# Optimization experiments

Measured on AMD Instinct MI355X. Metric: run time of the kernel, lower is better.

Reference implementation:

```python
import jax, jax.numpy as jnp
import numpy as np

N_NODES = 100_000
N_EDGES = 1_600_000
N_GRAPHS = 64
EPS = 1e-7  # GENConv message epsilon
D_IN, D_H, D_OUT, OUT_DIM = 128, 192, 128, 10


def _w(k, fan_in, fan_out):
    return jax.random.normal(k, (fan_in, fan_out), jnp.float32) * (1.0 / np.sqrt(fan_in))


def setup_inputs() -> dict:
    key = jax.random.key(0)
    ks = jax.random.split(key, 8)
    return {
        "x": jax.random.normal(ks[0], (N_NODES, D_IN), jnp.float32),
        "W0": _w(ks[1], D_IN, D_H), "b0": jnp.zeros((D_H,), jnp.float32),
        "W1": _w(ks[2], D_H, D_H), "b1": jnp.zeros((D_H,), jnp.float32),
        "W2": _w(ks[3], D_H, D_H), "b2": jnp.zeros((D_H,), jnp.float32),
        "W3": _w(ks[4], D_H, D_OUT), "b3": jnp.zeros((D_OUT,), jnp.float32),
        "Wfc": _w(ks[5], D_OUT, OUT_DIM), "bfc": jnp.zeros((OUT_DIM,), jnp.float32),
        "edge_index": jax.random.randint(ks[6], (2, N_EDGES), 0, N_NODES, jnp.int32),
        "batch": jnp.sort(jax.random.randint(ks[7], (N_NODES,), 0, N_GRAPHS, jnp.int32)),
    }


def _genconv(x, W, b, src, dst):
    # GENConv (num_layers=1, aggr='add'): message = relu(x_j) + eps,
    # scatter-add to dst, residual add, single Linear MLP.
    msg = jax.nn.relu(x[src]) + EPS          # [E, d]
    agg = jax.ops.segment_sum(msg, dst, num_segments=N_NODES)  # [N, d]
    return (x + agg) @ W + b


def reference(x, W0, b0, W1, b1, W2, b2, W3, b3, Wfc, bfc, edge_index, batch):
    src, dst = edge_index[0], edge_index[1]  # source_to_target flow
    for W, b in ((W0, b0), (W1, b1), (W2, b2), (W3, b3)):
        x = _genconv(x, W, b, src, dst)
    # global mean pool over graphs
    sums = jax.ops.segment_sum(x, batch, num_segments=N_GRAPHS)
    counts = jax.ops.segment_sum(jnp.ones((x.shape[0],), x.dtype), batch,
                                 num_segments=N_GRAPHS)
    pooled = sums / jnp.maximum(counts, 1.0)[:, None]  # [G, D_OUT]
    logits = pooled @ Wfc + bfc                        # [G, OUT_DIM]
    return jax.nn.log_softmax(logits, axis=1)
```

## Files before the change

### kernel.cpp

```cpp
#include <hip/hip_runtime.h>
#include <hip/hip_bf16.h>
#include <stdint.h>

constexpr int NN = 100000;
constexpr int NE = 1600000;
constexpr int NG = 64;
constexpr int S  = 192;
constexpr int NB_SCAN = 98;
constexpr unsigned int ZOFF = (unsigned int)NN * 384u;

constexpr int PREP_CONVX_BLK = 12500;
constexpr int PREP_INDEG_BLK = 1563;
constexpr int PREP_CONVW_BLK = 384;
constexpr int PREP_GB_BLK    = 391;
constexpr int PREP_GRID = PREP_CONVX_BLK + PREP_INDEG_BLK + PREP_CONVW_BLK + PREP_GB_BLK;

constexpr int EG_BLOCKS = 391;
constexpr int HROW = 50048;

typedef __bf16 bf16x8 __attribute__((ext_vector_type(8)));
typedef float  f32x16 __attribute__((ext_vector_type(16)));
typedef float  f32x2  __attribute__((ext_vector_type(2)));

union U16x4 { uint4 u; bf16x8 b; };

__device__ __forceinline__ float bl(unsigned int u) { return __uint_as_float(u << 16); }
__device__ __forceinline__ float bh(unsigned int u) { return __uint_as_float(u & 0xffff0000u); }
__device__ __forceinline__ float b16f(unsigned short u) { return __uint_as_float(((unsigned int)u) << 16); }
__device__ __forceinline__ unsigned int fb(float f) {
    unsigned int u = __float_as_uint(f);
    return (u + 0x7fffu + ((u >> 16) & 1u)) >> 16;
}
__device__ __forceinline__ unsigned int prelu(unsigned int u) {
    unsigned int r;
    asm("v_pk_max_f16 %0, %1, %2" : "=v"(r) : "v"(u), "v"(0u));
    return r;
}
__device__ __forceinline__ unsigned int cnt2bf(unsigned int h) {
    float f0 = (float)(h & 0xffffu);
    float f1 = (float)(h >> 16);
    return (__float_as_uint(f0) >> 16) | (__float_as_uint(f1) & 0xffff0000u);
}

__global__ __launch_bounds__(256) void k_prep(const float* __restrict__ x,
                                              const int* __restrict__ ei,
                                              const int* __restrict__ bat,
                                              const float* __restrict__ W0, const float* __restrict__ W1,
                                              const float* __restrict__ W2,
                                              unsigned short* __restrict__ A_,
                                              int* __restrict__ indeg, int* __restrict__ slot,
                                              unsigned short* __restrict__ T0, unsigned short* __restrict__ T1,
                                              unsigned short* __restrict__ T2,
                                              int* __restrict__ nstart) {
    const int b = blockIdx.x;
    if (b < PREP_CONVX_BLK) {
        int id = b * 256 + threadIdx.x;
        if (id < 96) ((unsigned int*)(A_ + (size_t)NN * S))[id] = 0u;
        int row = id >> 5, c4 = id & 31;
        float4 v = ((const float4*)x)[id];
        uint2 a;
        a.x = fb(v.x) | (fb(v.y) << 16);
        a.y = fb(v.z) | (fb(v.w) << 16);
        *(uint2*)(A_ + row * S + c4 * 4) = a;
    } else if (b < PREP_CONVX_BLK + PREP_INDEG_BLK) {
        int e4 = ((b - PREP_CONVX_BLK) * 256 + threadIdx.x) * 4;
        if (e4 < NE) {
            int4 d = *(const int4*)(ei + NE + e4);
            int4 sl;
            sl.x = atomicAdd(&indeg[d.x], 1);
            sl.y = atomicAdd(&indeg[d.y], 1);
            sl.z = atomicAdd(&indeg[d.z], 1);
            sl.w = atomicAdd(&indeg[d.w], 1);
            *(int4*)(slot + e4) = sl;
        }
    } else if (b < PREP_CONVX_BLK + PREP_INDEG_BLK + PREP_CONVW_BLK) {
        int id = (b - PREP_CONVX_BLK - PREP_INDEG_BLK) * 256 + threadIdx.x;
        const float* W; unsigned short* T; int N, base;
        if      (id < 24576) { W = W0; T = T0; N = 192; base = 0;     }
        else if (id < 61440) { W = W1; T = T1; N = 192; base = 24576; }
        else                 { W = W2; T = T2; N = 192; base = 61440; }
        int lid = id - base;
        int ci = lid >> 3, j = lid & 7;
        int kc = ci / N, n = ci % N;
        T[lid] = (unsigned short)fb(W[(kc * 8 + j) * N + n]);
    } else {
        int n = (b - PREP_CONVX_BLK - PREP_INDEG_BLK - PREP_CONVW_BLK) * 256 + threadIdx.x;
        if (n < NN) {
            int b0 = bat[n];
            int bprev = (n == 0) ? -1 : bat[n - 1];
            for (int g = bprev + 1; g <= b0; g++) nstart[g] = n;
            if (n == NN - 1)
                for (int g = b0 + 1; g < NG; g++) nstart[g] = NN;
        }
    }
}

__global__ __launch_bounds__(1024) void k_scan1(const int* __restrict__ indeg, int* __restrict__ offs,
                                                int* __restrict__ partials) {
    __shared__ int s[1024];
    int t = threadIdx.x;
    int gid = blockIdx.x * 1024 + t;
    int v = (gid < NN) ? indeg[gid] : 0;
    s[t] = v;
    __syncthreads();
    for (int d = 1; d < 1024; d <<= 1) {
        int tv = (t >= d) ? s[t - d] : 0;
        __syncthreads();
        s[t] += tv;
        __syncthreads();
    }
    if (gid < NN) offs[gid + 1] = s[t];
    if (t == 1023) partials[blockIdx.x] = s[1023];
}

__global__ __launch_bounds__(128) void k_scan2(int* __restrict__ offs, int* __restrict__ partials) {
    __shared__ int s[128];
    int t = threadIdx.x;
    int v = (t < NB_SCAN) ? partials[t] : 0;
    s[t] = v;
    __syncthreads();
    for (int d = 1; d < 128; d <<= 1) {
        int tv = (t >= d) ? s[t - d] : 0;
        __syncthreads();
        s[t] += tv;
        __syncthreads();
    }
    if (t < NB_SCAN) partials[t] = s[t] - v;
    if (t == 0) offs[0] = 0;
}

__global__ __launch_bounds__(1024) void k_scan3(int* __restrict__ offs, const int* __restrict__ partials) {
    int gid = blockIdx.x * 1024 + threadIdx.x;
    if (gid < NN) offs[gid + 1] += partials[blockIdx.x];
}

__global__ __launch_bounds__(256) void k_fill(const int* __restrict__ ei, const int* __restrict__ offs,
                                              const int* __restrict__ slot, int* __restrict__ csr) {
    int e4 = (blockIdx.x * 256 + threadIdx.x) * 4;
    if (e4 >= NE) return;
    int4 sv = *(const int4*)(ei + e4);
    int4 dv = *(const int4*)(ei + NE + e4);
    int4 sl = *(const int4*)(slot + e4);
    csr[offs[dv.x] + sl.x] = sv.x;
    csr[offs[dv.y] + sl.y] = sv.y;
    csr[offs[dv.z] + sl.z] = sv.z;
    csr[offs[dv.w] + sl.w] = sv.w;
}

__global__ __launch_bounds__(256, 8) void k_agg192(const unsigned short* __restrict__ Ain,
                                                   unsigned short* __restrict__ Yout,
                                                   const int* __restrict__ offs,
                                                   const int* __restrict__ indeg,
                                                   const int* __restrict__ csr) {
    const int w = threadIdx.x >> 6, lane = threadIdx.x & 63;
    const int i = __builtin_amdgcn_readfirstlane(blockIdx.x * 4 + w);
    const bool act = lane < 48;
    const int deg   = __builtin_amdgcn_readfirstlane(indeg[i]);
    const int start = __builtin_amdgcn_readfirstlane(offs[i]);
    const int fo = (act ? lane : 47) * 8;
    const char* Ab = (const char*)Ain;

    f32x2 A01, A23;
    {
        uint2 p = *(const uint2*)(Ab + (size_t)i * 384 + fo);
        const float ed = 1e-7f * (float)deg;
        A01 = (f32x2){bl(p.x) + ed, bh(p.x) + ed};
        A23 = (f32x2){bl(p.y) + ed, bh(p.y) + ed};
    }

    const int* ecsr = csr + start;
    for (int e = 0; e < deg; e += 16) {
        unsigned int off[16];
#pragma unroll
        for (int k = 0; k < 16; k++) {
            int v = ecsr[e + k];
            off[k] = (e + k < deg) ? (unsigned int)v * 384u : ZOFF;
        }
        uint2 p[16];
#pragma unroll
        for (int k = 0; k < 16; k++)
            p[k] = *(const uint2*)(Ab + (size_t)off[k] + fo);
#pragma unroll
        for (int k = 0; k < 16; k++) {
            unsigned int rx = prelu(p[k].x), ry = prelu(p[k].y);
            A01 += (f32x2){bl(rx), bh(rx)};
            A23 += (f32x2){bl(ry), bh(ry)};
        }
    }
    if (act) {
        uint2 o;
        o.x = fb(A01.x) | (fb(A01.y) << 16);
        o.y = fb(A23.x) | (fb(A23.y) << 16);
        *(uint2*)(Yout + (size_t)i * S + lane * 4) = o;
    }
}

__global__ __launch_bounds__(256, 8) void k_agg128(const unsigned short* __restrict__ Ain,
                                                   unsigned short* __restrict__ Yout,
                                                   const int* __restrict__ offs,
                                                   const int* __restrict__ indeg,
                                                   const int* __restrict__ csr) {
    const int w = threadIdx.x >> 6, lane = threadIdx.x & 63;
    const int i = __builtin_amdgcn_readfirstlane(blockIdx.x * 4 + w);
    const int deg   = __builtin_amdgcn_readfirstlane(indeg[i]);
    const int start = __builtin_amdgcn_readfirstlane(offs[i]);
    const int fo = lane * 4;
    const char* Ab = (const char*)Ain;

    f32x2 A01;
    {
        unsigned int p = *(const unsigned int*)(Ab + (size_t)i * 384 + fo);
        const float ed = 1e-7f * (float)deg;
        A01 = (f32x2){bl(p) + ed, bh(p) + ed};
    }

    const int* ecsr = csr + start;
    for (int e = 0; e < deg; e += 16) {
        unsigned int off[16];
#pragma unroll
        for (int k = 0; k < 16; k++) {
            int v = ecsr[e + k];
            off[k] = (e + k < deg) ? (unsigned int)v * 384u : ZOFF;
        }
        unsigned int q[16];
#pragma unroll
        for (int k = 0; k < 16; k++)
            q[k] = *(const unsigned int*)(Ab + (size_t)off[k] + fo);
#pragma unroll
        for (int k = 0; k < 16; k++) {
            unsigned int r = prelu(q[k]);
            A01 += (f32x2){bl(r), bh(r)};
        }
    }
    *(unsigned int*)(Yout + (size_t)i * S + lane * 2) =
        fb(A01.x) | (fb(A01.y) << 16);
}

template <int K, int N>
__global__ __launch_bounds__(256) void k_gemm(const unsigned short* __restrict__ Yin,
                                              const unsigned short* __restrict__ WtC,
                                              const float* __restrict__ bias,
                                              unsigned short* __restrict__ Aout) {
    static_assert(K % 16 == 0 && N % 32 == 0, "");
    const int w = threadIdx.x >> 6, lane = threadIdx.x & 63;
    const int rt = blockIdx.x * 4 + w;
    if (rt >= (NN / 32)) return;
    const int hl = lane >> 5, lr = lane & 31;
    const int row0 = rt * 32;
    f32x16 acc[N / 32];
#pragma unroll
    for (int c = 0; c < N / 32; c++)
#pragma unroll
        for (int r = 0; r < 16; r++) acc[c][r] = 0.f;

    const unsigned short* ap = Yin + (row0 + lr) * S + hl * 8;
    const uint4* b4 = (const uint4*)WtC;
#pragma unroll
    for (int ks = 0; ks < K / 16; ks++) {
        U16x4 a;
        a.u = *(const uint4*)(ap + ks * 16);
#pragma unroll
        for (int c = 0; c < N / 32; c++) {
            U16x4 b;
            b.u = b4[(ks * 2 + hl) * N + c * 32 + lr];
            acc[c] = __builtin_amdgcn_mfma_f32_32x32x16_bf16(a.b, b.b, acc[c], 0, 0, 0);
        }
    }
#pragma unroll
    for (int c = 0; c < N / 32; c++) {
        const int col = c * 32 + lr;
        const float bc = bias[col];
#pragma unroll
        for (int r = 0; r < 16; r++) {
            const int row = row0 + (r & 3) + 8 * (r >> 2) + 4 * hl;
            Aout[row * S + col] = (unsigned short)fb(acc[c][r] + bc);
        }
    }
}

__global__ __launch_bounds__(1024) void k_hist(const int* __restrict__ csr, const int* __restrict__ offs,
                                               const int* __restrict__ nstart,
                                               unsigned int* __restrict__ hist) {
    const int g = blockIdx.x;
    unsigned int* hrow = hist + (size_t)g * HROW;
    for (int i = threadIdx.x; i < HROW; i += 1024) hrow[i] = 0u;
    __syncthreads();
    const int s0 = offs[nstart[g]];
    const int s1 = (g == NG - 1) ? NE : offs[nstart[g + 1]];
    for (int p = s0 + threadIdx.x; p < s1; p += 1024) {
        int src = csr[p];
        atomicAdd(&hrow[src >> 1], 1u << (16 * (src & 1)));
    }
}

__global__ __launch_bounds__(384) void k_egemm(const unsigned short* __restrict__ A0,
                                               const unsigned int* __restrict__ hist,
                                               float* __restrict__ partials) {
    const int wv = threadIdx.x >> 6, lane = threadIdx.x & 63;
    const int b = blockIdx.x;
    const int j0 = b * 256;
    const int hl = lane >> 5, lr = lane & 31;
    const int feat = wv * 32 + lr;
    f32x16 acc[2];
#pragma unroll
    for (int m = 0; m < 2; m++)
#pragma unroll
        for (int r = 0; r < 16; r++) acc[m][r] = 0.f;

    for (int kk = 0; kk < 16; kk++) {
        const int jh = (j0 >> 1) + kk * 8 + hl * 4;
        U16x4 af[2];
#pragma unroll
        for (int m = 0; m < 2; m++) {
            uint4 h = *(const uint4*)(hist + (size_t)(m * 32 + lr) * HROW + jh);
            af[m].u = (uint4){cnt2bf(h.x), cnt2bf(h.y), cnt2bf(h.z), cnt2bf(h.w)};
        }
        U16x4 bf;
#pragma unroll
        for (int tp = 0; tp < 4; tp++) {
            int je = j0 + kk * 16 + hl * 8 + tp * 2;
            int ja = min(je, NN), jb = min(je + 1, NN);
            unsigned int u0 = A0[(size_t)ja * S + feat];
            unsigned int u1 = A0[(size_t)jb * S + feat];
            ((unsigned int*)&bf.u)[tp] = prelu(u0 | (u1 << 16));
        }
#pragma unroll
        for (int m = 0; m < 2; m++)
            acc[m] = __builtin_amdgcn_mfma_f32_32x32x16_bf16(af[m].b, bf.b, acc[m], 0, 0, 0);
    }
    float* pb = partials + (size_t)b * 12288;
#pragma unroll
    for (int m = 0; m < 2; m++)
#pragma unroll
        for (int r = 0; r < 16; r++) {
            const int g = m * 32 + (r & 3) + 8 * (r >> 2) + 4 * hl;
            pb[g * 192 + feat] = acc[m][r];
        }
}

__global__ __launch_bounds__(256) void k_reduce(const float* __restrict__ partials,
                                                float* __restrict__ msg) {
    int gf = blockIdx.x * 256 + threadIdx.x;
    if (gf >= 12288) return;
    float s = 0.f;
    for (int p = 0; p < EG_BLOCKS; p++)
        s += partials[(size_t)p * 12288 + gf];
    msg[gf] = s;
}

__global__ __launch_bounds__(192) void k_pool(const unsigned short* __restrict__ A_,
                                              const int* __restrict__ batch,
                                              const int* __restrict__ indeg,
                                              float* __restrict__ sums, float* __restrict__ cnt,
                                              float* __restrict__ degsum) {
    const int b = blockIdx.x;
    const int f = threadIdx.x;
    int n0 = b * 200;
    int n1 = min(n0 + 200, NN);
    int cur = batch[n0];
    float acc = 0.f;
    int run = 0, dacc = 0;
    for (int n = n0; n < n1; n++) {
        int g = batch[n];
        if (g != cur) {
            atomicAdd(&sums[cur * 192 + f], acc);
            if (f == 0) { atomicAdd(&cnt[cur], (float)run); atomicAdd(&degsum[cur], (float)dacc); }
            acc = 0.f; run = 0; dacc = 0; cur = g;
        }
        acc += b16f(A_[(size_t)n * S + f]);
        run++;
        if (f == 0) dacc += indeg[n];
    }
    atomicAdd(&sums[cur * 192 + f], acc);
    if (f == 0) { atomicAdd(&cnt[cur], (float)run); atomicAdd(&degsum[cur], (float)dacc); }
}

__global__ __launch_bounds__(128) void k_head(const float* __restrict__ sums, const float* __restrict__ msg,
                                              const float* __restrict__ cnt, const float* __restrict__ degsum,
                                              const float* __restrict__ W3, const float* __restrict__ b3,
                                              const float* __restrict__ Wfc, const float* __restrict__ bfc,
                                              float* __restrict__ out) {
    __shared__ float py[192];
    __shared__ float tl[128];
    __shared__ float lg[10];
    const int g = blockIdx.x, t = threadIdx.x;
    const float inv = 1.f / fmaxf(cnt[g], 1.f);
    const float ed = 1e-7f * degsum[g];
    for (int k = t; k < 192; k += 128)
        py[k] = (sums[g * 192 + k] + msg[g * 192 + k] + ed) * inv;
    __syncthreads();
    float tf = b3[t];
    for (int k = 0; k < 192; k++) tf += py[k] * W3[k * 128 + t];
    tl[t] = tf;
    __syncthreads();
    if (t < 10) {
        float s = bfc[t];
        for (int f = 0; f < 128; f++) s += tl[f] * Wfc[f * 10 + t];
        lg[t] = s;
    }
    __syncthreads();
    if (t < 10) {
        float m = lg[0];
        for (int k = 1; k < 10; k++) m = fmaxf(m, lg[k]);
        float se = 0.f;
        for (int k = 0; k < 10; k++) se += expf(lg[k] - m);
        out[g * 10 + t] = lg[t] - m - logf(se);
    }
}

constexpr size_t A0_OFF     = 0;
constexpr size_t A1_OFF     = 38400384;
constexpr size_t HIST_REL   = 0;
constexpr size_t PARTS_REL  = 12812288;
constexpr size_t CSR_OFF    = 76800384;
constexpr size_t OFFS_OFF   = 83200384;
constexpr size_t INDEG_OFF  = 83600512;
constexpr size_t SUMS_OFF   = 84000512;
constexpr size_t CNT_OFF    = 84049664;
constexpr size_t DEGS_OFF   = 84049920;
constexpr size_t PART_OFF   = 84050176;
constexpr size_t NSTART_OFF = 84050688;
constexpr size_t WT0_OFF    = 84050944;
constexpr size_t WT1_OFF    = 84100096;
constexpr size_t WT2_OFF    = 84173824;
constexpr size_t MSG_OFF    = 84247552;

extern "C" void kernel_launch(void* const* d_in, const int* in_sizes, int n_in,
                              void* d_out, int out_size, void* d_ws, size_t ws_size,
                              hipStream_t stream) {
    const float* x   = (const float*)d_in[0];
    const float* W0  = (const float*)d_in[1];
    const float* b0  = (const float*)d_in[2];
    const float* W1  = (const float*)d_in[3];
    const float* b1  = (const float*)d_in[4];
    const float* W2  = (const float*)d_in[5];
    const float* b2  = (const float*)d_in[6];
    const float* W3  = (const float*)d_in[7];
    const float* b3  = (const float*)d_in[8];
    const float* Wfc = (const float*)d_in[9];
    const float* bfc = (const float*)d_in[10];
    const int*   ei  = (const int*)d_in[11];
    const int*   bat = (const int*)d_in[12];
    float* out = (float*)d_out;

    char* ws = (char*)d_ws;
    unsigned short* A0  = (unsigned short*)(ws + A0_OFF);
    unsigned short* A1  = (unsigned short*)(ws + A1_OFF);
    int* slot   = (int*)(ws + A1_OFF);
    unsigned int* hist  = (unsigned int*)(ws + A1_OFF + HIST_REL);
    float* parts        = (float*)(ws + A1_OFF + PARTS_REL);
    int* csr    = (int*)(ws + CSR_OFF);
    int* offs   = (int*)(ws + OFFS_OFF);
    int* indeg  = (int*)(ws + INDEG_OFF);
    int* part   = (int*)(ws + PART_OFF);
    int* nstart = (int*)(ws + NSTART_OFF);
    unsigned short* Wt0 = (unsigned short*)(ws + WT0_OFF);
    unsigned short* Wt1 = (unsigned short*)(ws + WT1_OFF);
    unsigned short* Wt2 = (unsigned short*)(ws + WT2_OFF);
    float* sums   = (float*)(ws + SUMS_OFF);
    float* cnt    = (float*)(ws + CNT_OFF);
    float* degsum = (float*)(ws + DEGS_OFF);
    float* msg    = (float*)(ws + MSG_OFF);

    hipMemsetAsync(ws + INDEG_OFF, 0, 449664, stream);

    k_prep<<<PREP_GRID, 256, 0, stream>>>(x, ei, bat, W0, W1, W2, A0, indeg, slot,
                                          Wt0, Wt1, Wt2, nstart);

    k_scan1<<<NB_SCAN, 1024, 0, stream>>>(indeg, offs, part);
    k_scan2<<<1, 128, 0, stream>>>(offs, part);
    k_scan3<<<NB_SCAN, 1024, 0, stream>>>(offs, part);
    k_fill<<<(NE / 4 + 255) / 256, 256, 0, stream>>>(ei, offs, slot, csr);

    const int AGG_GRID  = NN / 4;
    const int GEMM_GRID = (NN / 32 + 3) / 4;

    k_agg128<<<AGG_GRID, 256, 0, stream>>>(A0, A1, offs, indeg, csr);
    k_gemm<128, 192><<<GEMM_GRID, 256, 0, stream>>>(A1, Wt0, b0, A0);
    k_agg192<<<AGG_GRID, 256, 0, stream>>>(A0, A1, offs, indeg, csr);
    k_gemm<192, 192><<<GEMM_GRID, 256, 0, stream>>>(A1, Wt1, b1, A0);
    k_agg192<<<AGG_GRID, 256, 0, stream>>>(A0, A1, offs, indeg, csr);
    k_gemm<192, 192><<<GEMM_GRID, 256, 0, stream>>>(A1, Wt2, b2, A0);

    k_hist<<<NG, 1024, 0, stream>>>(csr, offs, nstart, hist);
    k_egemm<<<EG_BLOCKS, 384, 0, stream>>>(A0, hist, parts);
    k_reduce<<<48, 256, 0, stream>>>(parts, msg);
    k_pool<<<500, 192, 0, stream>>>(A0, bat, indeg, sums, cnt, degsum);
    k_head<<<NG, 128, 0, stream>>>(sums, msg, cnt, degsum, W3, b3, Wfc, bfc, out);
}
```

Measured before the change: 717.8 us.

## Fuse neighbor aggregation with GEMM via LDS tile, merge hist and pool kernels

Each aggregation kernel and its following bf16 MFMA GEMM are merged into one kernel. Each block aggregates 96 nodes into an LDS tile and then multiplies it by the weights, so the intermediate Y buffer no longer round-trips through global memory and three launches go away. The scan3 pass is removed: the block partial is added on the fly wherever an offset is read. The histogram and pooling kernels are merged into one launch, with the histogram split across 4 blocks per graph. Buffers are ping-ponged between A0 and A1, so hist and parts now live in A0. The cost is lower occupancy from large blocks with LDS, and a serial per-wave aggregation of 16 rows before the MFMA phase.

```diff
diff --git a/kernel.cpp b/kernel.cpp
--- a/kernel.cpp
+++ b/kernel.cpp
@@ -17,6 +17,11 @@
 
 constexpr int EG_BLOCKS = 391;
 constexpr int HROW = 50048;
+constexpr int QROW = HROW / 4;
+
+constexpr int FB_NODES = 96;
+constexpr int FB_GRID  = (NN + FB_NODES - 1) / FB_NODES;
+constexpr int PS = 200;
 
 typedef __bf16 bf16x8 __attribute__((ext_vector_type(8)));
 typedef float  f32x16 __attribute__((ext_vector_type(16)));
@@ -48,6 +53,7 @@
                                               const float* __restrict__ W0, const float* __restrict__ W1,
                                               const float* __restrict__ W2,
                                               unsigned short* __restrict__ A_,
+                                              unsigned short* __restrict__ A1_,
                                               int* __restrict__ indeg, int* __restrict__ slot,
                                               unsigned short* __restrict__ T0, unsigned short* __restrict__ T1,
                                               unsigned short* __restrict__ T2,
@@ -55,7 +61,10 @@
     const int b = blockIdx.x;
     if (b < PREP_CONVX_BLK) {
         int id = b * 256 + threadIdx.x;
-        if (id < 96) ((unsigned int*)(A_ + (size_t)NN * S))[id] = 0u;
+        if (id < 192) {
+            unsigned short* Az = (id < 96) ? A_ : A1_;
+            ((unsigned int*)(Az + (size_t)NN * S))[id < 96 ? id : id - 96] = 0u;
+        }
         int row = id >> 5, c4 = id & 31;
         float4 v = ((const float4*)x)[id];
         uint2 a;
@@ -129,171 +138,196 @@
     if (t == 0) offs[0] = 0;
 }
 
-__global__ __launch_bounds__(1024) void k_scan3(int* __restrict__ offs, const int* __restrict__ partials) {
-    int gid = blockIdx.x * 1024 + threadIdx.x;
-    if (gid < NN) offs[gid + 1] += partials[blockIdx.x];
+__device__ __forceinline__ int toff(const int* __restrict__ offs, const int* __restrict__ part, int j) {
+    return j ? (offs[j] + part[(j - 1) >> 10]) : 0;
 }
 
 __global__ __launch_bounds__(256) void k_fill(const int* __restrict__ ei, const int* __restrict__ offs,
+                                              const int* __restrict__ part,
                                               const int* __restrict__ slot, int* __restrict__ csr) {
     int e4 = (blockIdx.x * 256 + threadIdx.x) * 4;
     if (e4 >= NE) return;
     int4 sv = *(const int4*)(ei + e4);
     int4 dv = *(const int4*)(ei + NE + e4);
     int4 sl = *(const int4*)(slot + e4);
-    csr[offs[dv.x] + sl.x] = sv.x;
-    csr[offs[dv.y] + sl.y] = sv.y;
-    csr[offs[dv.z] + sl.z] = sv.z;
-    csr[offs[dv.w] + sl.w] = sv.w;
-}
-
-__global__ __launch_bounds__(256, 8) void k_agg192(const unsigned short* __restrict__ Ain,
-                                                   unsigned short* __restrict__ Yout,
-                                                   const int* __restrict__ offs,
-                                                   const int* __restrict__ indeg,
-                                                   const int* __restrict__ csr) {
-    const int w = threadIdx.x >> 6, lane = threadIdx.x & 63;
-    const int i = __builtin_amdgcn_readfirstlane(blockIdx.x * 4 + w);
-    const bool act = lane < 48;
-    const int deg   = __builtin_amdgcn_readfirstlane(indeg[i]);
-    const int start = __builtin_amdgcn_readfirstlane(offs[i]);
-    const int fo = (act ? lane : 47) * 8;
+    csr[toff(offs, part, dv.x) + sl.x] = sv.x;
+    csr[toff(offs, part, dv.y) + sl.y] = sv.y;
+    csr[toff(offs, part, dv.z) + sl.z] = sv.z;
+    csr[toff(offs, part, dv.w) + sl.w] = sv.w;
+}
+
+template <int KF>
+__global__ __launch_bounds__(384, 6) void k_fusedag(const unsigned short* __restrict__ Ain,
+                                                    unsigned short* __restrict__ Aout,
+                                                    const int* __restrict__ offs,
+                                                    const int* __restrict__ part,
+                                                    const int* __restrict__ indeg,
+                                                    const int* __restrict__ csr,
+                                                    const unsigned short* __restrict__ WtC,
+                                                    const float* __restrict__ bias) {
+    __shared__ unsigned short yt[FB_NODES * PS];
+    const int wv = threadIdx.x >> 6, lane = threadIdx.x & 63;
+    const int base = __builtin_amdgcn_readfirstlane(blockIdx.x * FB_NODES);
     const char* Ab = (const char*)Ain;
 
-    f32x2 A01, A23;
-    {
-        uint2 p = *(const uint2*)(Ab + (size_t)i * 384 + fo);
-        const float ed = 1e-7f * (float)deg;
-        A01 = (f32x2){bl(p.x) + ed, bh(p.x) + ed};
-        A23 = (f32x2){bl(p.y) + ed, bh(p.y) + ed};
-    }
-
-    const int* ecsr = csr + start;
-    for (int e = 0; e < deg; e += 16) {
-        unsigned int off[16];
-#pragma unroll
-        for (int k = 0; k < 16; k++) {
-            int v = ecsr[e + k];
-            off[k] = (e + k < deg) ? (unsigned int)v * 384u : ZOFF;
-        }
-        uint2 p[16];
-#pragma unroll
-        for (int k = 0; k < 16; k++)
-            p[k] = *(const uint2*)(Ab + (size_t)off[k] + fo);
-#pragma unroll
-        for (int k = 0; k < 16; k++) {
-            unsigned int rx = prelu(p[k].x), ry = prelu(p[k].y);
-            A01 += (f32x2){bl(rx), bh(rx)};
-            A23 += (f32x2){bl(ry), bh(ry)};
-        }
-    }
-    if (act) {
-        uint2 o;
-        o.x = fb(A01.x) | (fb(A01.y) << 16);
-        o.y = fb(A23.x) | (fb(A23.y) << 16);
-        *(uint2*)(Yout + (size_t)i * S + lane * 4) = o;
-    }
-}
-
-__global__ __launch_bounds__(256, 8) void k_agg128(const unsigned short* __restrict__ Ain,
-                                                   unsigned short* __restrict__ Yout,
-                                                   const int* __restrict__ offs,
-                                                   const int* __restrict__ indeg,
-                                                   const int* __restrict__ csr) {
-    const int w = threadIdx.x >> 6, lane = threadIdx.x & 63;
-    const int i = __builtin_amdgcn_readfirstlane(blockIdx.x * 4 + w);
-    const int deg   = __builtin_amdgcn_readfirstlane(indeg[i]);
-    const int start = __builtin_amdgcn_readfirstlane(offs[i]);
-    const int fo = lane * 4;
-    const char* Ab = (const char*)Ain;
-
-    f32x2 A01;
-    {
-        unsigned int p = *(const unsigned int*)(Ab + (size_t)i * 384 + fo);
-        const float ed = 1e-7f * (float)deg;
-        A01 = (f32x2){bl(p) + ed, bh(p) + ed};
-    }
-
-    const int* ecsr = csr + start;
-    for (int e = 0; e < deg; e += 16) {
-        unsigned int off[16];
-#pragma unroll
-        for (int k = 0; k < 16; k++) {
-            int v = ecsr[e + k];
-            off[k] = (e + k < deg) ? (unsigned int)v * 384u : ZOFF;
-        }
-        unsigned int q[16];
-#pragma unroll
-        for (int k = 0; k < 16; k++)
-            q[k] = *(const unsigned int*)(Ab + (size_t)off[k] + fo);
-#pragma unroll
-        for (int k = 0; k < 16; k++) {
-            unsigned int r = prelu(q[k]);
-            A01 += (f32x2){bl(r), bh(r)};
-        }
-    }
-    *(unsigned int*)(Yout + (size_t)i * S + lane * 2) =
-        fb(A01.x) | (fb(A01.y) << 16);
-}
-
-template <int K, int N>
-__global__ __launch_bounds__(256) void k_gemm(const unsigned short* __restrict__ Yin,
-                                              const unsigned short* __restrict__ WtC,
-                                              const float* __restrict__ bias,
-                                              unsigned short* __restrict__ Aout) {
-    static_assert(K % 16 == 0 && N % 32 == 0, "");
-    const int w = threadIdx.x >> 6, lane = threadIdx.x & 63;
-    const int rt = blockIdx.x * 4 + w;
-    if (rt >= (NN / 32)) return;
+    for (int t = 0; t < 16; t++) {
+        const int lrow = wv * 16 + t;
+        const int i = __builtin_amdgcn_readfirstlane(base + lrow);
+        unsigned short* yrow = yt + lrow * PS;
+        if (i >= NN) {
+            if (KF == 192) { if (lane < 48) *(uint2*)((char*)yrow + lane * 8) = (uint2){0u, 0u}; }
+            else           { *(unsigned int*)((char*)yrow + lane * 4) = 0u; }
+            continue;
+        }
+        const int deg   = __builtin_amdgcn_readfirstlane(indeg[i]);
+        const int start = __builtin_amdgcn_readfirstlane(toff(offs, part, i));
+        const int* ecsr = csr + start;
+        if (KF == 192) {
+            const bool act = lane < 48;
+            const int fo = (act ? lane : 47) * 8;
+            f32x2 A01, A23;
+            {
+                uint2 p = *(const uint2*)(Ab + (size_t)i * 384 + fo);
+                const float ed = 1e-7f * (float)deg;
+                A01 = (f32x2){bl(p.x) + ed, bh(p.x) + ed};
+                A23 = (f32x2){bl(p.y) + ed, bh(p.y) + ed};
+            }
+            for (int e = 0; e < deg; e += 16) {
+                unsigned int off[16];
+#pragma unroll
+                for (int k = 0; k < 16; k++) {
+                    int v = ecsr[e + k];
+                    off[k] = (e + k < deg) ? (unsigned int)v * 384u : ZOFF;
+                }
+                uint2 p[16];
+#pragma unroll
+                for (int k = 0; k < 16; k++)
+                    p[k] = *(const uint2*)(Ab + (size_t)off[k] + fo);
+#pragma unroll
+                for (int k = 0; k < 16; k++) {
+                    unsigned int rx = prelu(p[k].x), ry = prelu(p[k].y);
+                    A01 += (f32x2){bl(rx), bh(rx)};
+                    A23 += (f32x2){bl(ry), bh(ry)};
+                }
+            }
+            if (act) {
+                uint2 o;
+                o.x = fb(A01.x) | (fb(A01.y) << 16);
+                o.y = fb(A23.x) | (fb(A23.y) << 16);
+                *(uint2*)((char*)yrow + lane * 8) = o;
+            }
+        } else {
+            const int fo = lane * 4;
+            f32x2 A01;
+            {
+                unsigned int p = *(const unsigned int*)(Ab + (size_t)i * 384 + fo);
+                const float ed = 1e-7f * (float)deg;
+                A01 = (f32x2){bl(p) + ed, bh(p) + ed};
+            }
+            for (int e = 0; e < deg; e += 16) {
+                unsigned int off[16];
+#pragma unroll
+                for (int k = 0; k < 16; k++) {
+                    int v = ecsr[e + k];
+                    off[k] = (e + k < deg) ? (unsigned int)v * 384u : ZOFF;
+                }
+                unsigned int q[16];
+#pragma unroll
+                for (int k = 0; k < 16; k++)
+                    q[k] = *(const unsigned int*)(Ab + (size_t)off[k] + fo);
+#pragma unroll
+                for (int k = 0; k < 16; k++) {
+                    unsigned int r = prelu(q[k]);
+                    A01 += (f32x2){bl(r), bh(r)};
+                }
+            }
+            *(unsigned int*)((char*)yrow + lane * 4) = fb(A01.x) | (fb(A01.y) << 16);
+        }
+    }
+    __syncthreads();
+
     const int hl = lane >> 5, lr = lane & 31;
-    const int row0 = rt * 32;
-    f32x16 acc[N / 32];
-#pragma unroll
-    for (int c = 0; c < N / 32; c++)
-#pragma unroll
-        for (int r = 0; r < 16; r++) acc[c][r] = 0.f;
-
-    const unsigned short* ap = Yin + (row0 + lr) * S + hl * 8;
+    const int ct = wv;
+    f32x16 acc[3];
+#pragma unroll
+    for (int rt = 0; rt < 3; rt++)
+#pragma unroll
+        for (int r = 0; r < 16; r++) acc[rt][r] = 0.f;
+
     const uint4* b4 = (const uint4*)WtC;
 #pragma unroll
-    for (int ks = 0; ks < K / 16; ks++) {
-        U16x4 a;
-        a.u = *(const uint4*)(ap + ks * 16);
-#pragma unroll
-        for (int c = 0; c < N / 32; c++) {
-            U16x4 b;
-            b.u = b4[(ks * 2 + hl) * N + c * 32 + lr];
-            acc[c] = __builtin_amdgcn_mfma_f32_32x32x16_bf16(a.b, b.b, acc[c], 0, 0, 0);
-        }
-    }
-#pragma unroll
-    for (int c = 0; c < N / 32; c++) {
-        const int col = c * 32 + lr;
-        const float bc = bias[col];
+    for (int ks = 0; ks < KF / 16; ks++) {
+        U16x4 b;
+        b.u = b4[(ks * 2 + hl) * 192 + ct * 32 + lr];
+#pragma unroll
+        for (int rt = 0; rt < 3; rt++) {
+            U16x4 a;
+            a.u = *(const uint4*)(yt + (rt * 32 + lr) * PS + ks * 16 + hl * 8);
+            acc[rt] = __builtin_amdgcn_mfma_f32_32x32x16_bf16(a.b, b.b, acc[rt], 0, 0, 0);
+        }
+    }
+    const int col = ct * 32 + lr;
+    const float bc = bias[col];
+#pragma unroll
+    for (int rt = 0; rt < 3; rt++)
 #pragma unroll
         for (int r = 0; r < 16; r++) {
-            const int row = row0 + (r & 3) + 8 * (r >> 2) + 4 * hl;
-            Aout[row * S + col] = (unsigned short)fb(acc[c][r] + bc);
-        }
-    }
-}
-
-__global__ __launch_bounds__(1024) void k_hist(const int* __restrict__ csr, const int* __restrict__ offs,
-                                               const int* __restrict__ nstart,
-                                               unsigned int* __restrict__ hist) {
-    const int g = blockIdx.x;
-    unsigned int* hrow = hist + (size_t)g * HROW;
-    for (int i = threadIdx.x; i < HROW; i += 1024) hrow[i] = 0u;
-    __syncthreads();
-    const int s0 = offs[nstart[g]];
-    const int s1 = (g == NG - 1) ? NE : offs[nstart[g + 1]];
-    for (int p = s0 + threadIdx.x; p < s1; p += 1024) {
-        int src = csr[p];
-        atomicAdd(&hrow[src >> 1], 1u << (16 * (src & 1)));
-    }
-}
-
-__global__ __launch_bounds__(384) void k_egemm(const unsigned short* __restrict__ A0,
+            const int row = base + rt * 32 + (r & 3) + 8 * (r >> 2) + 4 * hl;
+            if (row < NN) Aout[(size_t)row * S + col] = (unsigned short)fb(acc[rt][r] + bc);
+        }
+}
+
+__global__ __launch_bounds__(256) void k_histpool(const int* __restrict__ csr,
+                                                  const int* __restrict__ offs,
+                                                  const int* __restrict__ part,
+                                                  const int* __restrict__ nstart,
+                                                  unsigned int* __restrict__ hist,
+                                                  const unsigned short* __restrict__ X3,
+                                                  const int* __restrict__ bat,
+                                                  const int* __restrict__ indeg,
+                                                  float* __restrict__ sums, float* __restrict__ cnt,
+                                                  float* __restrict__ degsum) {
+    const int b = blockIdx.x;
+    if (b < 256) {
+        const int g = b >> 2, q = b & 3;
+        unsigned int* hrow = hist + (size_t)g * HROW;
+        const unsigned int q0 = q * QROW;
+        for (int i = threadIdx.x; i < QROW; i += 256) hrow[q0 + i] = 0u;
+        __syncthreads();
+        const int s0 = toff(offs, part, nstart[g]);
+        const int s1 = (g == NG - 1) ? NE : toff(offs, part, nstart[g + 1]);
+        for (int p = s0 + threadIdx.x; p < s1; p += 256) {
+            int src = csr[p];
+            unsigned int h = (unsigned int)src >> 1;
+            if (h - q0 < (unsigned int)QROW)
+                atomicAdd(&hrow[h], 1u << (16 * (src & 1)));
+        }
+    } else {
+        const int pb = b - 256;
+        const int f = threadIdx.x;
+        if (f >= 192) return;
+        int n0 = pb * 200;
+        int n1 = min(n0 + 200, NN);
+        int cur = bat[n0];
+        float acc = 0.f;
+        int run = 0, dacc = 0;
+        for (int n = n0; n < n1; n++) {
+            int g = bat[n];
+            if (g != cur) {
+                atomicAdd(&sums[cur * 192 + f], acc);
+                if (f == 0) { atomicAdd(&cnt[cur], (float)run); atomicAdd(&degsum[cur], (float)dacc); }
+                acc = 0.f; run = 0; dacc = 0; cur = g;
+            }
+            acc += b16f(X3[(size_t)n * S + f]);
+            run++;
+            if (f == 0) dacc += indeg[n];
+        }
+        atomicAdd(&sums[cur * 192 + f], acc);
+        if (f == 0) { atomicAdd(&cnt[cur], (float)run); atomicAdd(&degsum[cur], (float)dacc); }
+    }
+}
+
+__global__ __launch_bounds__(384) void k_egemm(const unsigned short* __restrict__ X3,
                                                const unsigned int* __restrict__ hist,
                                                float* __restrict__ partials) {
     const int wv = threadIdx.x >> 6, lane = threadIdx.x & 63;
@@ -320,8 +354,8 @@
         for (int tp = 0; tp < 4; tp++) {
             int je = j0 + kk * 16 + hl * 8 + tp * 2;
             int ja = min(je, NN), jb = min(je + 1, NN);
-            unsigned int u0 = A0[(size_t)ja * S + feat];
-            unsigned int u1 = A0[(size_t)jb * S + feat];
+            unsigned int u0 = X3[(size_t)ja * S + feat];
+            unsigned int u1 = X3[(size_t)jb * S + feat];
             ((unsigned int*)&bf.u)[tp] = prelu(u0 | (u1 << 16));
         }
 #pragma unroll
@@ -346,33 +380,6 @@
     for (int p = 0; p < EG_BLOCKS; p++)
         s += partials[(size_t)p * 12288 + gf];
     msg[gf] = s;
-}
-
-__global__ __launch_bounds__(192) void k_pool(const unsigned short* __restrict__ A_,
-                                              const int* __restrict__ batch,
-                                              const int* __restrict__ indeg,
-                                              float* __restrict__ sums, float* __restrict__ cnt,
-                                              float* __restrict__ degsum) {
-    const int b = blockIdx.x;
-    const int f = threadIdx.x;
-    int n0 = b * 200;
-    int n1 = min(n0 + 200, NN);
-    int cur = batch[n0];
-    float acc = 0.f;
-    int run = 0, dacc = 0;
-    for (int n = n0; n < n1; n++) {
-        int g = batch[n];
-        if (g != cur) {
-            atomicAdd(&sums[cur * 192 + f], acc);
-            if (f == 0) { atomicAdd(&cnt[cur], (float)run); atomicAdd(&degsum[cur], (float)dacc); }
-            acc = 0.f; run = 0; dacc = 0; cur = g;
-        }
-        acc += b16f(A_[(size_t)n * S + f]);
-        run++;
-        if (f == 0) dacc += indeg[n];
-    }
-    atomicAdd(&sums[cur * 192 + f], acc);
-    if (f == 0) { atomicAdd(&cnt[cur], (float)run); atomicAdd(&degsum[cur], (float)dacc); }
 }
 
 __global__ __launch_bounds__(128) void k_head(const float* __restrict__ sums, const float* __restrict__ msg,
@@ -412,18 +419,18 @@
 constexpr size_t A1_OFF     = 38400384;
 constexpr size_t HIST_REL   = 0;
 constexpr size_t PARTS_REL  = 12812288;
-constexpr size_t CSR_OFF    = 76800384;
-constexpr size_t OFFS_OFF   = 83200384;
-constexpr size_t INDEG_OFF  = 83600512;
-constexpr size_t SUMS_OFF   = 84000512;
-constexpr size_t CNT_OFF    = 84049664;
-constexpr size_t DEGS_OFF   = 84049920;
-constexpr size_t PART_OFF   = 84050176;
-constexpr size_t NSTART_OFF = 84050688;
-constexpr size_t WT0_OFF    = 84050944;
-constexpr size_t WT1_OFF    = 84100096;
-constexpr size_t WT2_OFF    = 84173824;
-constexpr size_t MSG_OFF    = 84247552;
+constexpr size_t CSR_OFF    = 76800768;
+constexpr size_t OFFS_OFF   = 83200768;
+constexpr size_t INDEG_OFF  = 83600896;
+constexpr size_t SUMS_OFF   = 84000896;
+constexpr size_t CNT_OFF    = 84050048;
+constexpr size_t DEGS_OFF   = 84050304;
+constexpr size_t PART_OFF   = 84050560;
+constexpr size_t NSTART_OFF = 84051072;
+constexpr size_t WT0_OFF    = 84051328;
+constexpr size_t WT1_OFF    = 84100480;
+constexpr size_t WT2_OFF    = 84174208;
+constexpr size_t MSG_OFF    = 84247936;
 
 extern "C" void kernel_launch(void* const* d_in, const int* in_sizes, int n_in,
                               void* d_out, int out_size, void* d_ws, size_t ws_size,
@@ -447,8 +454,8 @@
     unsigned short* A0  = (unsigned short*)(ws + A0_OFF);
     unsigned short* A1  = (unsigned short*)(ws + A1_OFF);
     int* slot   = (int*)(ws + A1_OFF);
-    unsigned int* hist  = (unsigned int*)(ws + A1_OFF + HIST_REL);
-    float* parts        = (float*)(ws + A1_OFF + PARTS_REL);
+    unsigned int* hist  = (unsigned int*)(ws + A0_OFF + HIST_REL);
+    float* parts        = (float*)(ws + A0_OFF + PARTS_REL);
     int* csr    = (int*)(ws + CSR_OFF);
     int* offs   = (int*)(ws + OFFS_OFF);
     int* indeg  = (int*)(ws + INDEG_OFF);
@@ -464,27 +471,20 @@
 
     hipMemsetAsync(ws + INDEG_OFF, 0, 449664, stream);
 
-    k_prep<<<PREP_GRID, 256, 0, stream>>>(x, ei, bat, W0, W1, W2, A0, indeg, slot,
+    k_prep<<<PREP_GRID, 256, 0, stream>>>(x, ei, bat, W0, W1, W2, A0, A1, indeg, slot,
                                           Wt0, Wt1, Wt2, nstart);
 
     k_scan1<<<NB_SCAN, 1024, 0, stream>>>(indeg, offs, part);
     k_scan2<<<1, 128, 0, stream>>>(offs, part);
-    k_scan3<<<NB_SCAN, 1024, 0, stream>>>(offs, part);
-    k_fill<<<(NE / 4 + 255) / 256, 256, 0, stream>>>(ei, offs, slot, csr);
-
-    const int AGG_GRID  = NN / 4;
-    const int GEMM_GRID = (NN / 32 + 3) / 4;
-
-    k_agg128<<<AGG_GRID, 256, 0, stream>>>(A0, A1, offs, indeg, csr);
-    k_gemm<128, 192><<<GEMM_GRID, 256, 0, stream>>>(A1, Wt0, b0, A0);
-    k_agg192<<<AGG_GRID, 256, 0, stream>>>(A0, A1, offs, indeg, csr);
-    k_gemm<192, 192><<<GEMM_GRID, 256, 0, stream>>>(A1, Wt1, b1, A0);
-    k_agg192<<<AGG_GRID, 256, 0, stream>>>(A0, A1, offs, indeg, csr);
-    k_gemm<192, 192><<<GEMM_GRID, 256, 0, stream>>>(A1, Wt2, b2, A0);
-
-    k_hist<<<NG, 1024, 0, stream>>>(csr, offs, nstart, hist);
-    k_egemm<<<EG_BLOCKS, 384, 0, stream>>>(A0, hist, parts);
+    k_fill<<<(NE / 4 + 255) / 256, 256, 0, stream>>>(ei, offs, part, slot, csr);
+
+    k_fusedag<128><<<FB_GRID, 384, 0, stream>>>(A0, A1, offs, part, indeg, csr, Wt0, b0);
+    k_fusedag<192><<<FB_GRID, 384, 0, stream>>>(A1, A0, offs, part, indeg, csr, Wt1, b1);
+    k_fusedag<192><<<FB_GRID, 384, 0, stream>>>(A0, A1, offs, part, indeg, csr, Wt2, b2);
+
+    k_histpool<<<756, 256, 0, stream>>>(csr, offs, part, nstart, hist, A1, bat, indeg,
+                                        sums, cnt, degsum);
+    k_egemm<<<EG_BLOCKS, 384, 0, stream>>>(A1, hist, parts);
     k_reduce<<<48, 256, 0, stream>>>(parts, msg);
-    k_pool<<<500, 192, 0, stream>>>(A0, bat, indeg, sums, cnt, degsum);
     k_head<<<NG, 128, 0, stream>>>(sums, msg, cnt, degsum, W3, b3, Wfc, bfc, out);
 }
```

After: 725.2 us. No clear change (+1.0%).

## Fold scan fix-up into consumers and fuse histogram with pooling kernel

Applied to the files above, without the earlier changes.

Removes the k_scan3 pass by having k_fill, the aggregation kernels and the histogram compute final CSR offsets on the fly as offs[j] plus the block partial. The per-graph histogram is split into four quarter-row blocks per graph for more parallelism, and the mean-pool kernel is merged into the same launch as extra blocks, dropping two launches. In exchange, every offset read costs an extra load and add, and each histogram block now scans its graph's whole edge range while keeping only a quarter of the entries, so edge reads are repeated four times.

```diff
diff --git a/kernel.cpp b/kernel.cpp
--- a/kernel.cpp
+++ b/kernel.cpp
@@ -17,6 +17,7 @@
 
 constexpr int EG_BLOCKS = 391;
 constexpr int HROW = 50048;
+constexpr int QROW = HROW / 4;
 
 typedef __bf16 bf16x8 __attribute__((ext_vector_type(8)));
 typedef float  f32x16 __attribute__((ext_vector_type(16)));
@@ -129,34 +130,35 @@
     if (t == 0) offs[0] = 0;
 }
 
-__global__ __launch_bounds__(1024) void k_scan3(int* __restrict__ offs, const int* __restrict__ partials) {
-    int gid = blockIdx.x * 1024 + threadIdx.x;
-    if (gid < NN) offs[gid + 1] += partials[blockIdx.x];
+__device__ __forceinline__ int toff(const int* __restrict__ offs, const int* __restrict__ part, int j) {
+    return j ? (offs[j] + part[(j - 1) >> 10]) : 0;
 }
 
 __global__ __launch_bounds__(256) void k_fill(const int* __restrict__ ei, const int* __restrict__ offs,
+                                              const int* __restrict__ part,
                                               const int* __restrict__ slot, int* __restrict__ csr) {
     int e4 = (blockIdx.x * 256 + threadIdx.x) * 4;
     if (e4 >= NE) return;
     int4 sv = *(const int4*)(ei + e4);
     int4 dv = *(const int4*)(ei + NE + e4);
     int4 sl = *(const int4*)(slot + e4);
-    csr[offs[dv.x] + sl.x] = sv.x;
-    csr[offs[dv.y] + sl.y] = sv.y;
-    csr[offs[dv.z] + sl.z] = sv.z;
-    csr[offs[dv.w] + sl.w] = sv.w;
+    csr[toff(offs, part, dv.x) + sl.x] = sv.x;
+    csr[toff(offs, part, dv.y) + sl.y] = sv.y;
+    csr[toff(offs, part, dv.z) + sl.z] = sv.z;
+    csr[toff(offs, part, dv.w) + sl.w] = sv.w;
 }
 
 __global__ __launch_bounds__(256, 8) void k_agg192(const unsigned short* __restrict__ Ain,
                                                    unsigned short* __restrict__ Yout,
                                                    const int* __restrict__ offs,
+                                                   const int* __restrict__ part,
                                                    const int* __restrict__ indeg,
                                                    const int* __restrict__ csr) {
     const int w = threadIdx.x >> 6, lane = threadIdx.x & 63;
     const int i = __builtin_amdgcn_readfirstlane(blockIdx.x * 4 + w);
     const bool act = lane < 48;
     const int deg   = __builtin_amdgcn_readfirstlane(indeg[i]);
-    const int start = __builtin_amdgcn_readfirstlane(offs[i]);
+    const int start = __builtin_amdgcn_readfirstlane(toff(offs, part, i));
     const int fo = (act ? lane : 47) * 8;
     const char* Ab = (const char*)Ain;
 
@@ -198,12 +200,13 @@
 __global__ __launch_bounds__(256, 8) void k_agg128(const unsigned short* __restrict__ Ain,
                                                    unsigned short* __restrict__ Yout,
                                                    const int* __restrict__ offs,
+                                                   const int* __restrict__ part,
                                                    const int* __restrict__ indeg,
                                                    const int* __restrict__ csr) {
     const int w = threadIdx.x >> 6, lane = threadIdx.x & 63;
     const int i = __builtin_amdgcn_readfirstlane(blockIdx.x * 4 + w);
     const int deg   = __builtin_amdgcn_readfirstlane(indeg[i]);
-    const int start = __builtin_amdgcn_readfirstlane(offs[i]);
+    const int start = __builtin_amdgcn_readfirstlane(toff(offs, part, i));
     const int fo = lane * 4;
     const char* Ab = (const char*)Ain;
 
@@ -278,22 +281,57 @@
     }
 }
 
-__global__ __launch_bounds__(1024) void k_hist(const int* __restrict__ csr, const int* __restrict__ offs,
-                                               const int* __restrict__ nstart,
-                                               unsigned int* __restrict__ hist) {
-    const int g = blockIdx.x;
-    unsigned int* hrow = hist + (size_t)g * HROW;
-    for (int i = threadIdx.x; i < HROW; i += 1024) hrow[i] = 0u;
-    __syncthreads();
-    const int s0 = offs[nstart[g]];
-    const int s1 = (g == NG - 1) ? NE : offs[nstart[g + 1]];
-    for (int p = s0 + threadIdx.x; p < s1; p += 1024) {
-        int src = csr[p];
-        atomicAdd(&hrow[src >> 1], 1u << (16 * (src & 1)));
-    }
-}
-
-__global__ __launch_bounds__(384) void k_egemm(const unsigned short* __restrict__ A0,
+__global__ __launch_bounds__(256) void k_histpool(const int* __restrict__ csr,
+                                                  const int* __restrict__ offs,
+                                                  const int* __restrict__ part,
+                                                  const int* __restrict__ nstart,
+                                                  unsigned int* __restrict__ hist,
+                                                  const unsigned short* __restrict__ X3,
+                                                  const int* __restrict__ bat,
+                                                  const int* __restrict__ indeg,
+                                                  float* __restrict__ sums, float* __restrict__ cnt,
+                                                  float* __restrict__ degsum) {
+    const int b = blockIdx.x;
+    if (b < 256) {
+        const int g = b >> 2, q = b & 3;
+        unsigned int* hrow = hist + (size_t)g * HROW;
+        const unsigned int q0 = q * QROW;
+        for (int i = threadIdx.x; i < QROW; i += 256) hrow[q0 + i] = 0u;
+        __syncthreads();
+        const int s0 = toff(offs, part, nstart[g]);
+        const int s1 = (g == NG - 1) ? NE : toff(offs, part, nstart[g + 1]);
+        for (int p = s0 + threadIdx.x; p < s1; p += 256) {
+            int src = csr[p];
+            unsigned int h = (unsigned int)src >> 1;
+            if (h - q0 < (unsigned int)QROW)
+                atomicAdd(&hrow[h], 1u << (16 * (src & 1)));
+        }
+    } else {
+        const int pb = b - 256;
+        const int f = threadIdx.x;
+        if (f >= 192) return;
+        int n0 = pb * 200;
+        int n1 = min(n0 + 200, NN);
+        int cur = bat[n0];
+        float acc = 0.f;
+        int run = 0, dacc = 0;
+        for (int n = n0; n < n1; n++) {
+            int g = bat[n];
+            if (g != cur) {
+                atomicAdd(&sums[cur * 192 + f], acc);
+                if (f == 0) { atomicAdd(&cnt[cur], (float)run); atomicAdd(&degsum[cur], (float)dacc); }
+                acc = 0.f; run = 0; dacc = 0; cur = g;
+            }
+            acc += b16f(X3[(size_t)n * S + f]);
+            run++;
+            if (f == 0) dacc += indeg[n];
+        }
+        atomicAdd(&sums[cur * 192 + f], acc);
+        if (f == 0) { atomicAdd(&cnt[cur], (float)run); atomicAdd(&degsum[cur], (float)dacc); }
+    }
+}
+
+__global__ __launch_bounds__(384) void k_egemm(const unsigned short* __restrict__ X3,
                                                const unsigned int* __restrict__ hist,
                                                float* __restrict__ partials) {
     const int wv = threadIdx.x >> 6, lane = threadIdx.x & 63;
@@ -320,8 +358,8 @@
         for (int tp = 0; tp < 4; tp++) {
             int je = j0 + kk * 16 + hl * 8 + tp * 2;
             int ja = min(je, NN), jb = min(je + 1, NN);
-            unsigned int u0 = A0[(size_t)ja * S + feat];
-            unsigned int u1 = A0[(size_t)jb * S + feat];
+            unsigned int u0 = X3[(size_t)ja * S + feat];
+            unsigned int u1 = X3[(size_t)jb * S + feat];
             ((unsigned int*)&bf.u)[tp] = prelu(u0 | (u1 << 16));
         }
 #pragma unroll
@@ -346,33 +384,6 @@
     for (int p = 0; p < EG_BLOCKS; p++)
         s += partials[(size_t)p * 12288 + gf];
     msg[gf] = s;
-}
-
-__global__ __launch_bounds__(192) void k_pool(const unsigned short* __restrict__ A_,
-                                              const int* __restrict__ batch,
-                                              const int* __restrict__ indeg,
-                                              float* __restrict__ sums, float* __restrict__ cnt,
-                                              float* __restrict__ degsum) {
-    const int b = blockIdx.x;
-    const int f = threadIdx.x;
-    int n0 = b * 200;
-    int n1 = min(n0 + 200, NN);
-    int cur = batch[n0];
-    float acc = 0.f;
-    int run = 0, dacc = 0;
-    for (int n = n0; n < n1; n++) {
-        int g = batch[n];
-        if (g != cur) {
-            atomicAdd(&sums[cur * 192 + f], acc);
-            if (f == 0) { atomicAdd(&cnt[cur], (float)run); atomicAdd(&degsum[cur], (float)dacc); }
-            acc = 0.f; run = 0; dacc = 0; cur = g;
-        }
-        acc += b16f(A_[(size_t)n * S + f]);
-        run++;
-        if (f == 0) dacc += indeg[n];
-    }
-    atomicAdd(&sums[cur * 192 + f], acc);
-    if (f == 0) { atomicAdd(&cnt[cur], (float)run); atomicAdd(&degsum[cur], (float)dacc); }
 }
 
 __global__ __launch_bounds__(128) void k_head(const float* __restrict__ sums, const float* __restrict__ msg,
@@ -469,22 +480,21 @@
 
     k_scan1<<<NB_SCAN, 1024, 0, stream>>>(indeg, offs, part);
     k_scan2<<<1, 128, 0, stream>>>(offs, part);
-    k_scan3<<<NB_SCAN, 1024, 0, stream>>>(offs, part);
-    k_fill<<<(NE / 4 + 255) / 256, 256, 0, stream>>>(ei, offs, slot, csr);
+    k_fill<<<(NE / 4 + 255) / 256, 256, 0, stream>>>(ei, offs, part, slot, csr);
 
     const int AGG_GRID  = NN / 4;
     const int GEMM_GRID = (NN / 32 + 3) / 4;
 
-    k_agg128<<<AGG_GRID, 256, 0, stream>>>(A0, A1, offs, indeg, csr);
+    k_agg128<<<AGG_GRID, 256, 0, stream>>>(A0, A1, offs, part, indeg, csr);
     k_gemm<128, 192><<<GEMM_GRID, 256, 0, stream>>>(A1, Wt0, b0, A0);
-    k_agg192<<<AGG_GRID, 256, 0, stream>>>(A0, A1, offs, indeg, csr);
+    k_agg192<<<AGG_GRID, 256, 0, stream>>>(A0, A1, offs, part, indeg, csr);
     k_gemm<192, 192><<<GEMM_GRID, 256, 0, stream>>>(A1, Wt1, b1, A0);
-    k_agg192<<<AGG_GRID, 256, 0, stream>>>(A0, A1, offs, indeg, csr);
+    k_agg192<<<AGG_GRID, 256, 0, stream>>>(A0, A1, offs, part, indeg, csr);
     k_gemm<192, 192><<<GEMM_GRID, 256, 0, stream>>>(A1, Wt2, b2, A0);
 
-    k_hist<<<NG, 1024, 0, stream>>>(csr, offs, nstart, hist);
+    k_histpool<<<756, 256, 0, stream>>>(csr, offs, part, nstart, hist, A0, bat, indeg,
+                                        sums, cnt, degsum);
     k_egemm<<<EG_BLOCKS, 384, 0, stream>>>(A0, hist, parts);
     k_reduce<<<48, 256, 0, stream>>>(parts, msg);
-    k_pool<<<500, 192, 0, stream>>>(A0, bat, indeg, sums, cnt, degsum);
     k_head<<<NG, 128, 0, stream>>>(sums, msg, cnt, degsum, W3, b3, Wfc, bfc, out);
 }
```

Result: faster. 671.2 us (-6.5%).
